# Performance work log

Measured on AMD Instinct MI355X. Metric: run time of the kernel, lower is better.

The kernel has to match this reference:

```python
import jax, jax.numpy as jnp
import numpy as np

D_MODEL = 256
N_HEADS = 8
D_FFN = 1024
B, N = 4, 1024
HEAD_DIM = D_MODEL // N_HEADS
LN_EPS = 1e-5


def _ln(x, g, b):
    mu = jnp.mean(x, axis=-1, keepdims=True)
    var = jnp.var(x, axis=-1, keepdims=True)
    return (x - mu) * jax.lax.rsqrt(var + LN_EPS) * g + b


def setup_inputs() -> dict:
    key = jax.random.key(0)
    ks = jax.random.split(key, 16)
    s = 0.02
    return {
        "embed": jax.random.normal(ks[0], (B, N, D_MODEL), jnp.float32),
        "refer_bbox": jax.random.uniform(ks[1], (B, N, 4), jnp.float32),
        "dist": jax.random.uniform(ks[2], (B, N, N), jnp.float32),
        "query_pos": jax.random.normal(ks[3], (B, N, D_MODEL), jnp.float32),
        "in_proj_w": jax.random.normal(ks[4], (3 * D_MODEL, D_MODEL), jnp.float32) * s,
        "in_proj_b": jnp.zeros((3 * D_MODEL,), jnp.float32),
        "out_w": jax.random.normal(ks[5], (D_MODEL, D_MODEL), jnp.float32) * s,
        "out_b": jnp.zeros((D_MODEL,), jnp.float32),
        "tau_w": jax.random.normal(ks[6], (N_HEADS, D_MODEL), jnp.float32) * s,
        "tau_b": jax.random.uniform(ks[7], (N_HEADS,), jnp.float32, 0.0, 2.0),
        "w1": jax.random.normal(ks[8], (D_FFN, D_MODEL), jnp.float32) * s,
        "b1": jnp.zeros((D_FFN,), jnp.float32),
        "w2": jax.random.normal(ks[9], (D_MODEL, D_FFN), jnp.float32) * s,
        "b2": jnp.zeros((D_MODEL,), jnp.float32),
        "g1": jnp.ones((D_MODEL,), jnp.float32),
        "beta1": jnp.zeros((D_MODEL,), jnp.float32),
        "g2": jnp.ones((D_MODEL,), jnp.float32),
        "beta2": jnp.zeros((D_MODEL,), jnp.float32),
    }


def reference(embed, refer_bbox, dist, query_pos, in_proj_w, in_proj_b, out_w, out_b,
              tau_w, tau_b, w1, b1, w2, b2, g1, beta1, g2, beta2):
    # tau: (B, N, H) -> (B, H, N); additive bias mask[b,h,i,j] = dist[b,i,j] * tau[b,h,i]
    tau = (embed @ tau_w.T + tau_b).transpose(0, 2, 1)
    bias = dist[:, None, :, :] * tau[..., None]  # (B, H, N, N)

    qk = embed + query_pos  # q = k = embed + pos, v = embed
    wq, wk, wv = jnp.split(in_proj_w, 3, axis=0)
    bq, bk, bv = jnp.split(in_proj_b, 3, axis=0)
    q = (qk @ wq.T + bq).reshape(B, N, N_HEADS, HEAD_DIM)
    k = (qk @ wk.T + bk).reshape(B, N, N_HEADS, HEAD_DIM)
    v = (embed @ wv.T + bv).reshape(B, N, N_HEADS, HEAD_DIM)

    scores = jnp.einsum("bihd,bjhd->bhij", q, k) / np.sqrt(HEAD_DIM) + bias
    attn = jax.nn.softmax(scores, axis=-1)
    ctx = jnp.einsum("bhij,bjhd->bihd", attn, v).reshape(B, N, D_MODEL)
    tgt = ctx @ out_w.T + out_b

    x = _ln(embed + tgt, g1, beta1)
    ffn = jax.nn.relu(x @ w1.T + b1) @ w2.T + b2
    return _ln(x + ffn, g2, beta2)
```

## Files before the change

kernel.cpp:

```cpp
#include <hip/hip_runtime.h>
#include <math.h>

#define D_MODEL 256
#define N_HEADS 8
#define HEAD_DIM 32
#define D_FFN   1024
#define BB      4
#define NN      1024
#define M_TOT   (BB * NN)
#define LN_EPS  1e-5f

#define QSCALE_LOG2E 0.2550348612f
#define LOG2E        1.4426950408889634f

typedef float f32x4 __attribute__((ext_vector_type(4)));
typedef short bf16x8 __attribute__((ext_vector_type(8)));

__device__ __forceinline__ unsigned short f2bf(float f) {
    unsigned int u = __float_as_uint(f);
    unsigned int r = (u + 0x7fffu + ((u >> 16) & 1u)) >> 16;
    return (unsigned short)r;
}
__device__ __forceinline__ ushort4 pack4(float4 v) {
    ushort4 o; o.x = f2bf(v.x); o.y = f2bf(v.y); o.z = f2bf(v.z); o.w = f2bf(v.w);
    return o;
}
__device__ __forceinline__ float fast_exp2(float x) {
#if __has_builtin(__builtin_amdgcn_exp2f)
    return __builtin_amdgcn_exp2f(x);
#else
    return exp2f(x);
#endif
}
__device__ __forceinline__ float bf2f(unsigned short s) {
    return __uint_as_float(((unsigned int)s) << 16);
}

__global__ __launch_bounds__(256)
void prep_all_kernel(const float4* __restrict__ e, const float4* __restrict__ qp,
                     ushort4* __restrict__ ebf, ushort4* __restrict__ qkbf,
                     const float4* __restrict__ inw, const float4* __restrict__ outw,
                     const float4* __restrict__ w1, const float4* __restrict__ w2,
                     const float4* __restrict__ tauw,
                     ushort4* __restrict__ o_inw, ushort4* __restrict__ o_outw,
                     ushort4* __restrict__ o_w1, ushort4* __restrict__ o_w2,
                     ushort4* __restrict__ o_taupad) {
    if (blockIdx.x < 1024) {
        int i = blockIdx.x * 256 + threadIdx.x;
        float4 ev = e[i], pv = qp[i];
        ebf[i] = pack4(ev);
        float4 s = make_float4(ev.x + pv.x, ev.y + pv.y, ev.z + pv.z, ev.w + pv.w);
        qkbf[i] = pack4(s);
    } else {
        int i = (blockIdx.x - 1024) * 256 + threadIdx.x;
        if (i < 49152)       o_inw[i] = pack4(inw[i]);
        else if (i < 65536)  o_outw[i - 49152] = pack4(outw[i - 49152]);
        else if (i < 131072) o_w1[i - 65536] = pack4(w1[i - 65536]);
        else if (i < 196608) o_w2[i - 131072] = pack4(w2[i - 131072]);
        else if (i < 200704) {
            int q = i - 196608;
            if (q < 512) o_taupad[q] = pack4(tauw[q]);
            else { ushort4 z = {0, 0, 0, 0}; o_taupad[q] = z; }
        }
    }
}

__global__ __launch_bounds__(256)
void qkv_mfma_kernel(const unsigned short* __restrict__ qk_bf,
                     const unsigned short* __restrict__ emb_bf,
                     const unsigned short* __restrict__ inw_bf,
                     const unsigned short* __restrict__ taupad,
                     const float* __restrict__ in_proj_b, const float* __restrict__ tau_b,
                     unsigned short* __restrict__ qb, unsigned short* __restrict__ kb,
                     unsigned short* __restrict__ vbT, float* __restrict__ taub) {
    const int w    = threadIdx.x >> 6;
    const int lane = threadIdx.x & 63;
    const int l16 = lane & 15, l4 = lane >> 4;
    const int n0 = blockIdx.x * 64;
    const int m0 = blockIdx.y * 64;
    const int wm = (w >> 1) * 32, wn = (w & 1) * 32;

    const unsigned short* A = (blockIdx.x < 8) ? qk_bf : emb_bf;
    const unsigned short* W0 = (n0 < 768) ? &inw_bf[(size_t)(n0 + wn + l16) * D_MODEL]
                                          : &taupad[(size_t)(wn + l16) * D_MODEL];
    const unsigned short* Ar0 = &A[(size_t)(m0 + wm + l16) * D_MODEL];

    f32x4 acc[2][2] = {};
    #pragma unroll
    for (int k0 = 0; k0 < D_MODEL; k0 += 32) {
        bf16x8 a0 = *(const bf16x8*)&Ar0[k0 + l4 * 8];
        bf16x8 a1 = *(const bf16x8*)&Ar0[16 * D_MODEL + k0 + l4 * 8];
        bf16x8 b0 = *(const bf16x8*)&W0[k0 + l4 * 8];
        bf16x8 b1 = *(const bf16x8*)&W0[16 * D_MODEL + k0 + l4 * 8];
        acc[0][0] = __builtin_amdgcn_mfma_f32_16x16x32_bf16(a0, b0, acc[0][0], 0, 0, 0);
        acc[0][1] = __builtin_amdgcn_mfma_f32_16x16x32_bf16(a0, b1, acc[0][1], 0, 0, 0);
        acc[1][0] = __builtin_amdgcn_mfma_f32_16x16x32_bf16(a1, b0, acc[1][0], 0, 0, 0);
        acc[1][1] = __builtin_amdgcn_mfma_f32_16x16x32_bf16(a1, b1, acc[1][1], 0, 0, 0);
    }

    #pragma unroll
    for (int i = 0; i < 2; i++) {
        #pragma unroll
        for (int j = 0; j < 2; j++) {
            #pragma unroll
            for (int r = 0; r < 4; r++) {
                const int m = m0 + wm + i * 16 + l4 * 4 + r;
                const int b = m >> 10, nrow = m & 1023;
                const int c = n0 + wn + j * 16 + l16;
                float v = acc[i][j][r];
                if (c < 256) {
                    v = (v + in_proj_b[c]) * QSCALE_LOG2E;
                    int h = c >> 5, d = c & 31;
                    qb[((size_t)(b * N_HEADS + h) * NN + nrow) * HEAD_DIM + d] = f2bf(v);
                } else if (c < 512) {
                    v += in_proj_b[c];
                    int cc = c - 256; int h = cc >> 5, d = cc & 31;
                    kb[((size_t)(b * N_HEADS + h) * NN + nrow) * HEAD_DIM + d] = f2bf(v);
                } else if (c < 768) {
                    v += in_proj_b[c];
                    int cc = c - 512; int h = cc >> 5, d = cc & 31;
                    vbT[((size_t)(b * N_HEADS + h) * HEAD_DIM + d) * NN + nrow] = f2bf(v);
                } else if (c < 776) {
                    v = (v + tau_b[c - 768]) * LOG2E;
                    taub[(size_t)(b * N_HEADS + (c - 768)) * NN + nrow] = v;
                }
            }
        }
    }
}

__global__ __launch_bounds__(256)
void attn_mfma_kernel(const unsigned short* __restrict__ qb,
                      const unsigned short* __restrict__ kb,
                      const unsigned short* __restrict__ vbT,
                      const float* __restrict__ taub,
                      const float* __restrict__ dist,
                      unsigned short* __restrict__ Opart,
                      float* __restrict__ lpart) {
    __shared__ unsigned short Kf[4][4][512];
    __shared__ unsigned short Vf[4][2][2][512];
    __shared__ unsigned short Plds[4][16 * 72];
    const int w    = threadIdx.x >> 6;
    const int lane = threadIdx.x & 63;
    const int l16  = lane & 15;
    const int l4   = lane >> 4;
    const int bh = blockIdx.y;
    const int b = bh >> 3;
    const int z = blockIdx.z;
    const int i0 = blockIdx.x * 64 + w * 16;
    const int jbase = z * 256;

    {
        const int kt = w;
        const unsigned short* kb_z = &kb[((size_t)bh * NN + jbase + kt * 64) * HEAD_DIM];
        #pragma unroll
        for (int s = 0; s < 4; s++) {
            bf16x8 kv = *(const bf16x8*)&kb_z[(size_t)(l16 * 4 + s) * HEAD_DIM + l4 * 8];
            *(bf16x8*)&Kf[kt][s][lane * 8] = kv;
        }
        const unsigned short* vb_z = &vbT[(size_t)bh * HEAD_DIM * NN + jbase + kt * 64];
        #pragma unroll
        for (int c = 0; c < 2; c++)
            #pragma unroll
            for (int h2 = 0; h2 < 2; h2++) {
                bf16x8 vv = *(const bf16x8*)&vb_z[(size_t)(h2 * 16 + l16) * NN + c * 32 + l4 * 8];
                *(bf16x8*)&Vf[kt][c][h2][lane * 8] = vv;
            }
    }

    const f32x4 zero = {0.f, 0.f, 0.f, 0.f};
    bf16x8 qf = *(const bf16x8*)&qb[((size_t)bh * NN + i0 + l16) * HEAD_DIM + l4 * 8];
    float tau_r[4];
    const float* drow[4];
    #pragma unroll
    for (int r = 0; r < 4; r++) {
        tau_r[r] = taub[(size_t)bh * NN + i0 + l4 * 4 + r];
        drow[r] = &dist[((size_t)b * NN + i0 + l4 * 4 + r) * NN + jbase];
    }
    float l_acc[4] = {0.f, 0.f, 0.f, 0.f};
    f32x4 O0 = zero, O1 = zero;
    unsigned short* pw = &Plds[w][0];

    __syncthreads();

    for (int kt = 0; kt < 4; kt++) {
        const int j0 = kt * 64;
        f32x4 dd4[4];
        #pragma unroll
        for (int r = 0; r < 4; r++)
            dd4[r] = *(const f32x4*)&drow[r][j0 + l16 * 4];

        float parr[4][4];
        #pragma unroll
        for (int s = 0; s < 4; s++) {
            bf16x8 kfr = *(const bf16x8*)&Kf[kt][s][lane * 8];
            f32x4 S = __builtin_amdgcn_mfma_f32_16x16x32_bf16(qf, kfr, zero, 0, 0, 0);
            #pragma unroll
            for (int r = 0; r < 4; r++) {
                const float p = fast_exp2(S[r] + dd4[r][s] * tau_r[r]);
                parr[s][r] = p;
                l_acc[r] += p;
            }
        }

        #pragma unroll
        for (int r = 0; r < 4; r++) {
            ushort4 pk;
            pk.x = f2bf(parr[0][r]); pk.y = f2bf(parr[1][r]);
            pk.z = f2bf(parr[2][r]); pk.w = f2bf(parr[3][r]);
            *(ushort4*)&pw[(l4 * 4 + r) * 72 + l16 * 4] = pk;
        }
        asm volatile("s_waitcnt lgkmcnt(0)" ::: "memory");
        #pragma unroll
        for (int c = 0; c < 2; c++) {
            bf16x8 pf = *(const bf16x8*)&pw[l16 * 72 + c * 32 + l4 * 8];
            bf16x8 v0 = *(const bf16x8*)&Vf[kt][c][0][lane * 8];
            bf16x8 v1 = *(const bf16x8*)&Vf[kt][c][1][lane * 8];
            O0 = __builtin_amdgcn_mfma_f32_16x16x32_bf16(pf, v0, O0, 0, 0, 0);
            O1 = __builtin_amdgcn_mfma_f32_16x16x32_bf16(pf, v1, O1, 0, 0, 0);
        }
    }

    #pragma unroll
    for (int msk = 1; msk < 16; msk <<= 1)
        #pragma unroll
        for (int r = 0; r < 4; r++)
            l_acc[r] += __shfl_xor(l_acc[r], msk, 16);

    #pragma unroll
    for (int r = 0; r < 4; r++) {
        const int i = i0 + l4 * 4 + r;
        unsigned short* crow = &Opart[((size_t)(z * 32 + bh) * NN + i) * 32];
        crow[l16]      = f2bf(O0[r]);
        crow[16 + l16] = f2bf(O1[r]);
        if (l16 == 0)
            lpart[(size_t)(z * 32 + bh) * NN + i] = l_acc[r];
    }
}

__global__ __launch_bounds__(1024)
void post_kernel(const unsigned short* __restrict__ Opart, const float* __restrict__ lpart,
                 const unsigned short* __restrict__ outw,
                 const float* __restrict__ out_b, const float* __restrict__ embed,
                 const float* __restrict__ g1, const float* __restrict__ beta1,
                 const unsigned short* __restrict__ w1, const float* __restrict__ b1,
                 const unsigned short* __restrict__ w2, const float* __restrict__ b2,
                 const float* __restrict__ g2, const float* __restrict__ beta2,
                 float* __restrict__ out) {
    __shared__ float Lh[16][8];
    __shared__ unsigned short cs[16][264];
    __shared__ unsigned short xs[16][264];
    __shared__ unsigned short fs[16][1032];
    __shared__ float sums[16][4][4][2];

    const int tid = threadIdx.x;
    const int w = tid >> 6, lane = tid & 63;
    const int l16 = lane & 15, l4 = lane >> 4;
    const int m0 = blockIdx.x * 16;
    const int b = m0 >> 10;

    if (tid < 128) {
        const int row = tid >> 3, h = tid & 7;
        const int i = (m0 + row) & 1023;
        const int rowA = ((b * 8 + h) << 10) + i;
        float l = 0.f;
        #pragma unroll
        for (int z = 0; z < 4; z++) l += lpart[z * 32768 + rowA];
        Lh[row][h] = 1.0f / l;
    }
    __syncthreads();

    if (tid < 512) {
        const int row = tid >> 5;
        const int d0 = (tid & 31) * 8;
        const int h = d0 >> 5;
        const int dd = d0 & 31;
        const int i = (m0 + row) & 1023;
        const int rowA = ((b * 8 + h) << 10) + i;
        float s[8] = {};
        #pragma unroll
        for (int z = 0; z < 4; z++) {
            bf16x8 u = *(const bf16x8*)&Opart[((size_t)(z * 32768 + rowA)) * 32 + dd];
            #pragma unroll
            for (int j = 0; j < 8; j++) s[j] += bf2f((unsigned short)u[j]);
        }
        const float li = Lh[row][h];
        #pragma unroll
        for (int j = 0; j < 8; j++)
            cs[row][d0 + j] = f2bf(s[j] * li);
    }
    __syncthreads();

    const int cA = w * 16 + l16;
    f32x4 a0 = {}, a1 = {};
    {
        const unsigned short* wr = &outw[(size_t)cA * D_MODEL];
        #pragma unroll
        for (int kk = 0; kk < 4; kk++) {
            const int k0 = kk * 32, k1 = 128 + kk * 32;
            bf16x8 x0 = *(const bf16x8*)&cs[l16][k0 + l4 * 8];
            bf16x8 b0 = *(const bf16x8*)&wr[k0 + l4 * 8];
            bf16x8 x1 = *(const bf16x8*)&cs[l16][k1 + l4 * 8];
            bf16x8 b1v = *(const bf16x8*)&wr[k1 + l4 * 8];
            a0 = __builtin_amdgcn_mfma_f32_16x16x32_bf16(x0, b0, a0, 0, 0, 0);
            a1 = __builtin_amdgcn_mfma_f32_16x16x32_bf16(x1, b1v, a1, 0, 0, 0);
        }
    }
    float xv[4];
    {
        float s_r[4] = {0.f, 0.f, 0.f, 0.f}, q_r[4] = {0.f, 0.f, 0.f, 0.f};
        const float bs = out_b[cA];
        #pragma unroll
        for (int r = 0; r < 4; r++) {
            const int m = m0 + l4 * 4 + r;
            const float t = a0[r] + a1[r] + bs + embed[(size_t)m * D_MODEL + cA];
            xv[r] = t; s_r[r] += t; q_r[r] += t * t;
        }
        #pragma unroll
        for (int msk = 1; msk < 16; msk <<= 1)
            #pragma unroll
            for (int r = 0; r < 4; r++) {
                s_r[r] += __shfl_xor(s_r[r], msk, 16);
                q_r[r] += __shfl_xor(q_r[r], msk, 16);
            }
        if (l16 == 0)
            #pragma unroll
            for (int r = 0; r < 4; r++) {
                sums[w][l4][r][0] = s_r[r];
                sums[w][l4][r][1] = q_r[r];
            }
    }
    __syncthreads();
    #pragma unroll
    for (int r = 0; r < 4; r++) {
        float s = 0.f, q = 0.f;
        #pragma unroll
        for (int ww = 0; ww < 16; ww++) { s += sums[ww][l4][r][0]; q += sums[ww][l4][r][1]; }
        const float mu = s * (1.0f / D_MODEL);
        const float var = q * (1.0f / D_MODEL) - mu * mu;
        const float rstd = rsqrtf(var + LN_EPS);
        const float ov = (xv[r] - mu) * rstd * g1[cA] + beta1[cA];
        xv[r] = ov;
        xs[l4 * 4 + r][cA] = f2bf(ov);
    }
    __syncthreads();

    f32x4 accB[4] = {};
    {
        bf16x8 wf[4], wfn[4];
        #pragma unroll
        for (int j = 0; j < 4; j++)
            wf[j] = *(const bf16x8*)&w1[(size_t)(w * 64 + j * 16 + l16) * D_MODEL + l4 * 8];
        #pragma unroll
        for (int kk = 0; kk < 8; kk++) {
            const int k0 = kk * 32;
            if (kk < 7) {
                #pragma unroll
                for (int j = 0; j < 4; j++)
                    wfn[j] = *(const bf16x8*)&w1[(size_t)(w * 64 + j * 16 + l16) * D_MODEL + k0 + 32 + l4 * 8];
            }
            bf16x8 a = *(const bf16x8*)&xs[l16][k0 + l4 * 8];
            #pragma unroll
            for (int j = 0; j < 4; j++)
                accB[j] = __builtin_amdgcn_mfma_f32_16x16x32_bf16(a, wf[j], accB[j], 0, 0, 0);
            if (kk < 7) {
                #pragma unroll
                for (int j = 0; j < 4; j++) wf[j] = wfn[j];
            }
        }
    }
    #pragma unroll
    for (int j = 0; j < 4; j++) {
        const int fc = w * 64 + j * 16 + l16;
        const float bs = b1[fc];
        #pragma unroll
        for (int r = 0; r < 4; r++)
            fs[l4 * 4 + r][fc] = f2bf(fmaxf(accB[j][r] + bs, 0.f));
    }
    __syncthreads();

    f32x4 c0 = {}, c1 = {};
    {
        const unsigned short* wr = &w2[(size_t)cA * D_FFN];
        bf16x8 wb0 = *(const bf16x8*)&wr[l4 * 8];
        bf16x8 wb1 = *(const bf16x8*)&wr[512 + l4 * 8];
        #pragma unroll
        for (int kk = 0; kk < 16; kk++) {
            const int k0 = kk * 32, k1 = 512 + kk * 32;
            bf16x8 cur0 = wb0, cur1 = wb1;
            if (kk < 15) {
                wb0 = *(const bf16x8*)&wr[k0 + 32 + l4 * 8];
                wb1 = *(const bf16x8*)&wr[k1 + 32 + l4 * 8];
            }
            bf16x8 f0 = *(const bf16x8*)&fs[l16][k0 + l4 * 8];
            bf16x8 f1 = *(const bf16x8*)&fs[l16][k1 + l4 * 8];
            c0 = __builtin_amdgcn_mfma_f32_16x16x32_bf16(f0, cur0, c0, 0, 0, 0);
            c1 = __builtin_amdgcn_mfma_f32_16x16x32_bf16(f1, cur1, c1, 0, 0, 0);
        }
    }
    float v2[4];
    {
        float s_r[4] = {0.f, 0.f, 0.f, 0.f}, q_r[4] = {0.f, 0.f, 0.f, 0.f};
        const float bs = b2[cA];
        #pragma unroll
        for (int r = 0; r < 4; r++) {
            const float t = c0[r] + c1[r] + bs + xv[r];
            v2[r] = t; s_r[r] += t; q_r[r] += t * t;
        }
        #pragma unroll
        for (int msk = 1; msk < 16; msk <<= 1)
            #pragma unroll
            for (int r = 0; r < 4; r++) {
                s_r[r] += __shfl_xor(s_r[r], msk, 16);
                q_r[r] += __shfl_xor(q_r[r], msk, 16);
            }
        if (l16 == 0)
            #pragma unroll
            for (int r = 0; r < 4; r++) {
                sums[w][l4][r][0] = s_r[r];
                sums[w][l4][r][1] = q_r[r];
            }
    }
    __syncthreads();
    #pragma unroll
    for (int r = 0; r < 4; r++) {
        float s = 0.f, q = 0.f;
        #pragma unroll
        for (int ww = 0; ww < 16; ww++) { s += sums[ww][l4][r][0]; q += sums[ww][l4][r][1]; }
        const float mu = s * (1.0f / D_MODEL);
        const float var = q * (1.0f / D_MODEL) - mu * mu;
        const float rstd = rsqrtf(var + LN_EPS);
        const int m = m0 + l4 * 4 + r;
        out[(size_t)m * D_MODEL + cA] = (v2[r] - mu) * rstd * g2[cA] + beta2[cA];
    }
}

extern "C" void kernel_launch(void* const* d_in, const int* in_sizes, int n_in,
                              void* d_out, int out_size, void* d_ws, size_t ws_size,
                              hipStream_t stream) {
    const float* embed     = (const float*)d_in[0];
    const float* dist      = (const float*)d_in[2];
    const float* query_pos = (const float*)d_in[3];
    const float* in_proj_w = (const float*)d_in[4];
    const float* in_proj_b = (const float*)d_in[5];
    const float* out_w     = (const float*)d_in[6];
    const float* out_b     = (const float*)d_in[7];
    const float* tau_w     = (const float*)d_in[8];
    const float* tau_b     = (const float*)d_in[9];
    const float* w1        = (const float*)d_in[10];
    const float* b1        = (const float*)d_in[11];
    const float* w2        = (const float*)d_in[12];
    const float* b2        = (const float*)d_in[13];
    const float* g1        = (const float*)d_in[14];
    const float* beta1     = (const float*)d_in[15];
    const float* g2        = (const float*)d_in[16];
    const float* beta2     = (const float*)d_in[17];
    float* out = (float*)d_out;

    char* ws = (char*)d_ws;
    const size_t MB = 1024 * 1024;
    const size_t KB = 1024;
    unsigned short* emb_bf  = (unsigned short*)(ws);
    unsigned short* qk_bf   = (unsigned short*)(ws + 2 * MB);
    unsigned short* qb      = (unsigned short*)(ws + 4 * MB);
    unsigned short* kb      = (unsigned short*)(ws + 6 * MB);
    unsigned short* vbT     = (unsigned short*)(ws + 8 * MB);
    float*          taub    = (float*)(ws + 10 * MB);
    unsigned short* inw_bf  = (unsigned short*)(ws + 11 * MB);
    unsigned short* outw_bf = (unsigned short*)(ws + 11 * MB + 512 * KB);
    unsigned short* w1_bf   = (unsigned short*)(ws + 12 * MB);
    unsigned short* w2_bf   = (unsigned short*)(ws + 12 * MB + 512 * KB);
    unsigned short* taupad  = (unsigned short*)(ws + 13 * MB);
    unsigned short* Opart   = (unsigned short*)(ws + 14 * MB);
    float*          lpart   = (float*)(ws + 22 * MB);

    prep_all_kernel<<<dim3(1808), dim3(256), 0, stream>>>(
        (const float4*)embed, (const float4*)query_pos,
        (ushort4*)emb_bf, (ushort4*)qk_bf,
        (const float4*)in_proj_w, (const float4*)out_w, (const float4*)w1,
        (const float4*)w2, (const float4*)tau_w,
        (ushort4*)inw_bf, (ushort4*)outw_bf, (ushort4*)w1_bf, (ushort4*)w2_bf,
        (ushort4*)taupad);

    qkv_mfma_kernel<<<dim3(13, M_TOT / 64), dim3(256), 0, stream>>>(
        qk_bf, emb_bf, inw_bf, taupad, in_proj_b, tau_b, qb, kb, vbT, taub);

    attn_mfma_kernel<<<dim3(NN / 64, BB * N_HEADS, 4), dim3(256), 0, stream>>>(
        qb, kb, vbT, taub, dist, Opart, lpart);

    post_kernel<<<dim3(M_TOT / 16), dim3(1024), 0, stream>>>(
        Opart, lpart, outw_bf, out_b, embed, g1, beta1,
        w1_bf, b1, w2_bf, b2, g2, beta2, out);
}
```

Baseline: 180.8 us.

## Stage V transpose through LDS and prefetch FFN weights before barriers

In the QKV kernel, V-projection blocks now write their tile into a padded shared buffer and then emit the transposed vbT rows as contiguous 16-byte stores, replacing scattered 2-byte strided writes. In the output/FFN kernel, the partial-output reduction is spread across all threads with 4-wide loads instead of half the threads doing 8-wide loads. The first w1 and w2 weight fragments are loaded earlier, ahead of the LayerNorm and ReLU stages and their barriers, to hide global load latency. This adds LDS use and register pressure in exchange.

```diff
diff --git a/kernel.cpp b/kernel.cpp
--- a/kernel.cpp
+++ b/kernel.cpp
@@ -73,12 +73,14 @@
                      const float* __restrict__ in_proj_b, const float* __restrict__ tau_b,
                      unsigned short* __restrict__ qb, unsigned short* __restrict__ kb,
                      unsigned short* __restrict__ vbT, float* __restrict__ taub) {
+    __shared__ unsigned short vt[64][72];
     const int w    = threadIdx.x >> 6;
     const int lane = threadIdx.x & 63;
     const int l16 = lane & 15, l4 = lane >> 4;
     const int n0 = blockIdx.x * 64;
     const int m0 = blockIdx.y * 64;
     const int wm = (w >> 1) * 32, wn = (w & 1) * 32;
+    const bool isv = (blockIdx.x >= 8) && (blockIdx.x < 12);
 
     const unsigned short* A = (blockIdx.x < 8) ? qk_bf : emb_bf;
     const unsigned short* W0 = (n0 < 768) ? &inw_bf[(size_t)(n0 + wn + l16) * D_MODEL]
@@ -96,6 +98,30 @@
         acc[0][1] = __builtin_amdgcn_mfma_f32_16x16x32_bf16(a0, b1, acc[0][1], 0, 0, 0);
         acc[1][0] = __builtin_amdgcn_mfma_f32_16x16x32_bf16(a1, b0, acc[1][0], 0, 0, 0);
         acc[1][1] = __builtin_amdgcn_mfma_f32_16x16x32_bf16(a1, b1, acc[1][1], 0, 0, 0);
+    }
+
+    if (isv) {
+        #pragma unroll
+        for (int i = 0; i < 2; i++)
+            #pragma unroll
+            for (int j = 0; j < 2; j++) {
+                const int cl = wn + j * 16 + l16;
+                const float bs = in_proj_b[n0 + cl];
+                #pragma unroll
+                for (int r = 0; r < 4; r++)
+                    vt[cl][wm + i * 16 + l4 * 4 + r] = f2bf(acc[i][j][r] + bs);
+            }
+        __syncthreads();
+        const int t = threadIdx.x;
+        const int cl = t >> 2, q4 = t & 3;
+        const int cc = n0 + cl - 512;
+        const int h = cc >> 5, d = cc & 31;
+        const int b = m0 >> 10;
+        const int nrow0 = (m0 & 1023) + q4 * 16;
+        unsigned short* dst = &vbT[((size_t)(b * N_HEADS + h) * HEAD_DIM + d) * NN + nrow0];
+        *(uint4*)dst       = *(const uint4*)&vt[cl][q4 * 16];
+        *(uint4*)(dst + 8) = *(const uint4*)&vt[cl][q4 * 16 + 8];
+        return;
     }
 
     #pragma unroll
@@ -116,10 +142,6 @@
                     v += in_proj_b[c];
                     int cc = c - 256; int h = cc >> 5, d = cc & 31;
                     kb[((size_t)(b * N_HEADS + h) * NN + nrow) * HEAD_DIM + d] = f2bf(v);
-                } else if (c < 768) {
-                    v += in_proj_b[c];
-                    int cc = c - 512; int h = cc >> 5, d = cc & 31;
-                    vbT[((size_t)(b * N_HEADS + h) * HEAD_DIM + d) * NN + nrow] = f2bf(v);
                 } else if (c < 776) {
                     v = (v + tau_b[c - 768]) * LOG2E;
                     taub[(size_t)(b * N_HEADS + (c - 768)) * NN + nrow] = v;
@@ -270,24 +292,24 @@
     }
     __syncthreads();
 
-    if (tid < 512) {
-        const int row = tid >> 5;
-        const int d0 = (tid & 31) * 8;
+    {
+        const int row = tid >> 6;
+        const int d0 = (tid & 63) * 4;
         const int h = d0 >> 5;
         const int dd = d0 & 31;
         const int i = (m0 + row) & 1023;
         const int rowA = ((b * 8 + h) << 10) + i;
-        float s[8] = {};
+        float s[4] = {};
         #pragma unroll
         for (int z = 0; z < 4; z++) {
-            bf16x8 u = *(const bf16x8*)&Opart[((size_t)(z * 32768 + rowA)) * 32 + dd];
-            #pragma unroll
-            for (int j = 0; j < 8; j++) s[j] += bf2f((unsigned short)u[j]);
+            ushort4 u = *(const ushort4*)&Opart[((size_t)(z * 32768 + rowA)) * 32 + dd];
+            s[0] += bf2f(u.x); s[1] += bf2f(u.y); s[2] += bf2f(u.z); s[3] += bf2f(u.w);
         }
         const float li = Lh[row][h];
-        #pragma unroll
-        for (int j = 0; j < 8; j++)
-            cs[row][d0 + j] = f2bf(s[j] * li);
+        ushort4 o;
+        o.x = f2bf(s[0] * li); o.y = f2bf(s[1] * li);
+        o.z = f2bf(s[2] * li); o.w = f2bf(s[3] * li);
+        *(ushort4*)&cs[row][d0] = o;
     }
     __syncthreads();
 
@@ -306,6 +328,11 @@
             a1 = __builtin_amdgcn_mfma_f32_16x16x32_bf16(x1, b1v, a1, 0, 0, 0);
         }
     }
+    bf16x8 wf[4];
+    #pragma unroll
+    for (int j = 0; j < 4; j++)
+        wf[j] = *(const bf16x8*)&w1[(size_t)(w * 64 + j * 16 + l16) * D_MODEL + l4 * 8];
+
     float xv[4];
     {
         float s_r[4] = {0.f, 0.f, 0.f, 0.f}, q_r[4] = {0.f, 0.f, 0.f, 0.f};
@@ -347,10 +374,7 @@
 
     f32x4 accB[4] = {};
     {
-        bf16x8 wf[4], wfn[4];
-        #pragma unroll
-        for (int j = 0; j < 4; j++)
-            wf[j] = *(const bf16x8*)&w1[(size_t)(w * 64 + j * 16 + l16) * D_MODEL + l4 * 8];
+        bf16x8 wfn[4];
         #pragma unroll
         for (int kk = 0; kk < 8; kk++) {
             const int k0 = kk * 32;
@@ -369,6 +393,10 @@
             }
         }
     }
+    const unsigned short* wr2 = &w2[(size_t)cA * D_FFN];
+    bf16x8 wb0 = *(const bf16x8*)&wr2[l4 * 8];
+    bf16x8 wb1 = *(const bf16x8*)&wr2[512 + l4 * 8];
+
     #pragma unroll
     for (int j = 0; j < 4; j++) {
         const int fc = w * 64 + j * 16 + l16;
@@ -381,16 +409,13 @@
 
     f32x4 c0 = {}, c1 = {};
     {
-        const unsigned short* wr = &w2[(size_t)cA * D_FFN];
-        bf16x8 wb0 = *(const bf16x8*)&wr[l4 * 8];
-        bf16x8 wb1 = *(const bf16x8*)&wr[512 + l4 * 8];
         #pragma unroll
         for (int kk = 0; kk < 16; kk++) {
             const int k0 = kk * 32, k1 = 512 + kk * 32;
             bf16x8 cur0 = wb0, cur1 = wb1;
             if (kk < 15) {
-                wb0 = *(const bf16x8*)&wr[k0 + 32 + l4 * 8];
-                wb1 = *(const bf16x8*)&wr[k1 + 32 + l4 * 8];
+                wb0 = *(const bf16x8*)&wr2[k0 + 32 + l4 * 8];
+                wb1 = *(const bf16x8*)&wr2[k1 + 32 + l4 * 8];
             }
             bf16x8 f0 = *(const bf16x8*)&fs[l16][k0 + l4 * 8];
             bf16x8 f1 = *(const bf16x8*)&fs[l16][k1 + l4 * 8];
```

After: 181.9 us. About the same (+0.6%).
